# Kernel optimization log

Hardware: AMD Instinct MI355X
Metric: run time of the kernel (lower is better)

The kernel has to match this reference:

```python
import jax, jax.numpy as jnp
import numpy as np

B, H, W, C = 8, 128, 128, 256
IC = C // 8  # im_ch
INF_VAL = 3.4e38  # note: the original ADDS +INF on the H-axis diagonal (as in source)


def setup_inputs() -> dict:
    key = jax.random.key(0)
    ks = jax.random.split(key, 8)
    x = jax.random.normal(ks[0], (B, H, W, C), dtype=jnp.float32)
    s = 1.0 / np.sqrt(C).astype(np.float32)
    Wf = jax.random.normal(ks[1], (C, IC), dtype=jnp.float32) * s
    bf = jnp.zeros((IC,), dtype=jnp.float32)
    Wg = jax.random.normal(ks[2], (C, IC), dtype=jnp.float32) * s
    bg = jnp.zeros((IC,), dtype=jnp.float32)
    Wh = jax.random.normal(ks[3], (C, C), dtype=jnp.float32) * s
    bh = jnp.zeros((C,), dtype=jnp.float32)
    gamma = jnp.float32(0.5)  # source inits to 0.0; use 0.5 so output != x for testing
    return {"x": x, "Wf": Wf, "bf": bf, "Wg": Wg, "bg": bg, "Wh": Wh, "bh": bh, "gamma": gamma}


def reference(x, Wf, bf, Wg, bg, Wh, bh, gamma):
    b, h, w, c = x.shape
    # 1x1 convs == per-pixel GEMMs
    fx = jnp.einsum('bhwc,ck->bhwk', x, Wf) + bf   # [B,H,W,IC]
    gx = jnp.einsum('bhwc,ck->bhwk', x, Wg) + bg   # [B,H,W,IC]
    hx = jnp.einsum('bhwc,cd->bhwd', x, Wh) + bh   # [B,H,W,C]
    # H-axis energy: eh[b,i,w,j] = <fx[b,i,w,:], gx[b,j,w,:]> + INF on i==j diagonal
    eye_bias = (INF_VAL * jnp.eye(h, dtype=x.dtype))[:, None, :]  # [H,1,H] -> broadcast over w
    eh = jnp.einsum('biwk,bjwk->biwj', fx, gx) + eye_bias          # [B,H,W,H]
    # W-axis energy: ew[b,h,i,j] = <fx[b,h,i,:], gx[b,h,j,:]>
    ew = jnp.einsum('bhik,bhjk->bhij', fx, gx)                     # [B,H,W,W]
    # joint softmax over concatenated H+W axis
    att = jax.nn.softmax(jnp.concatenate([eh, ew], axis=-1), axis=-1)  # [B,H,W,H+W]
    att_h, att_w = att[..., :h], att[..., h:]
    # aggregate values along column (H) and row (W)
    out_h = jnp.einsum('biwj,bjwc->biwc', att_h, hx)  # [B,H,W,C]
    out_w = jnp.einsum('bhij,bhjc->bhic', att_w, hx)  # [B,H,W,C]
    return gamma * (out_h + out_w) + x
```

## Files before the change

### kernel.cpp

```cpp
#include <hip/hip_runtime.h>
#include <hip/hip_bf16.h>

typedef __attribute__((ext_vector_type(8))) short bf16x8;
typedef __attribute__((ext_vector_type(4))) float f32x4;

__device__ __forceinline__ unsigned f2bf(float f) {
    union { float f; unsigned u; } v; v.f = f;
    unsigned u = v.u;
    return (u + 0x7FFFu + ((u >> 16) & 1u)) >> 16;
}

__global__ void prep_whT(const float* __restrict__ Wh, ushort* __restrict__ whT) {
    int n = blockIdx.x;
    int k = threadIdx.x;
    whT[n * 256 + k] = (ushort)f2bf(Wh[k * 256 + n]);
}

__global__ __launch_bounds__(256, 4) void ccsa_gemm(
    const float* __restrict__ x, const ushort* __restrict__ whT,
    const float* __restrict__ bh, const float* __restrict__ gamma,
    float* __restrict__ out)
{
    __shared__ char lds[32768];
    const int tid  = threadIdx.x;
    const int lane = tid & 63;
    const int wv   = tid >> 6;
    const int r15  = lane & 15;
    const int g    = lane >> 4;
    const int swz  = (r15 & 7) << 4;

    const long row0 = (long)blockIdx.x * 64;
    const float* xblk = x + row0 * 256;

#pragma unroll
    for (int p = 0; p < 8; ++p) {
        int lin = p * 2048 + tid * 8;
        int r = lin >> 8;
        int c = lin & 255;
        float4 a0 = *(const float4*)(xblk + lin);
        float4 a1 = *(const float4*)(xblk + lin + 4);
        uint4 pk;
        pk.x = f2bf(a0.x) | (f2bf(a0.y) << 16);
        pk.y = f2bf(a0.z) | (f2bf(a0.w) << 16);
        pk.z = f2bf(a1.x) | (f2bf(a1.y) << 16);
        pk.w = f2bf(a1.z) | (f2bf(a1.w) << 16);
        int addr = r * 512 + ((c * 2) ^ ((r & 7) << 4));
        *(uint4*)(lds + addr) = pk;
    }

    const ushort* bp0 = whT + (wv * 64 +  0 + r15) * 256 + g * 8;
    const ushort* bp1 = whT + (wv * 64 + 16 + r15) * 256 + g * 8;
    const ushort* bp2 = whT + (wv * 64 + 32 + r15) * 256 + g * 8;
    const ushort* bp3 = whT + (wv * 64 + 48 + r15) * 256 + g * 8;

    __syncthreads();

    f32x4 acc[4][4] = {};

#pragma unroll
    for (int ksl = 0; ksl < 8; ++ksl) {
        bf16x8 bc[4];
        bc[0] = *(const bf16x8*)(bp0 + ksl * 32);
        bc[1] = *(const bf16x8*)(bp1 + ksl * 32);
        bc[2] = *(const bf16x8*)(bp2 + ksl * 32);
        bc[3] = *(const bf16x8*)(bp3 + ksl * 32);

        const int ko = (ksl * 64 + g * 16) ^ swz;
        bf16x8 af[4];
#pragma unroll
        for (int mi = 0; mi < 4; ++mi)
            af[mi] = *(const bf16x8*)(lds + (mi * 16 + r15) * 512 + ko);

#pragma unroll
        for (int mi = 0; mi < 4; ++mi)
#pragma unroll
            for (int ni = 0; ni < 4; ++ni)
                acc[mi][ni] = __builtin_amdgcn_mfma_f32_16x16x32_bf16(
                    af[mi], bc[ni], acc[mi][ni], 0, 0, 0);
    }

    const float gm = gamma[0];
    float bias[4];
#pragma unroll
    for (int ni = 0; ni < 4; ++ni) bias[ni] = bh[wv * 64 + ni * 16 + r15];

#pragma unroll
    for (int mi = 0; mi < 4; ++mi) {
#pragma unroll
        for (int rr = 0; rr < 4; ++rr) {
            int row = mi * 16 + g * 4 + rr;
#pragma unroll
            for (int ni = 0; ni < 4; ++ni) {
                int col2 = wv * 128 + ni * 32 + r15 * 2;
                int addr = row * 512 + (col2 ^ ((row & 7) << 4));
                ushort xv = *(const ushort*)(lds + addr);
                float xf = __uint_as_float(((unsigned)xv) << 16);
                float val = gm * (acc[mi][ni][rr] + bias[ni]) + xf;
                out[(row0 + row) * 256 + wv * 64 + ni * 16 + r15] = val;
            }
        }
    }
}

extern "C" void kernel_launch(void* const* d_in, const int* in_sizes, int n_in,
                              void* d_out, int out_size, void* d_ws, size_t ws_size,
                              hipStream_t stream) {
    const float* x  = (const float*)d_in[0];
    const float* Wh = (const float*)d_in[5];
    const float* bh = (const float*)d_in[6];
    const float* gm = (const float*)d_in[7];
    float* out = (float*)d_out;
    ushort* whT = (ushort*)d_ws;

    prep_whT<<<256, 256, 0, stream>>>(Wh, whT);
    ccsa_gemm<<<2048, 256, 0, stream>>>(x, whT, bh, gm, out);
}
```

Before: 70.70 us.

## Make GEMM kernel persistent with register prefetch and vectorized nontemporal stores

Converts the per-tile GEMM launch into a persistent grid where each block loops over several 64-row tiles, prefetching the next tile of x into registers while computing the current one. Swaps MFMA operand order so each lane owns four consecutive output columns, enabling float4 nontemporal stores instead of scalar stores. Also flips the weight-transpose prep indexing so global reads coalesce. The prefetch raises register pressure (launch bounds lowered) and the grid may leave some CUs with uneven tile counts.

Measured after the change: 221.9 us. +213.9%, slower.

```diff
diff --git a/kernel.cpp b/kernel.cpp
--- a/kernel.cpp
+++ b/kernel.cpp
@@ -1,22 +1,23 @@
 #include <hip/hip_runtime.h>
-#include <hip/hip_bf16.h>
 
 typedef __attribute__((ext_vector_type(8))) short bf16x8;
 typedef __attribute__((ext_vector_type(4))) float f32x4;
 
 __device__ __forceinline__ unsigned f2bf(float f) {
     union { float f; unsigned u; } v; v.f = f;
-    unsigned u = v.u;
-    return (u + 0x7FFFu + ((u >> 16) & 1u)) >> 16;
+    return (v.u + 0x7FFFu + ((v.u >> 16) & 1u)) >> 16;
 }
 
 __global__ void prep_whT(const float* __restrict__ Wh, ushort* __restrict__ whT) {
-    int n = blockIdx.x;
-    int k = threadIdx.x;
+    int k = blockIdx.x;
+    int n = threadIdx.x;
     whT[n * 256 + k] = (ushort)f2bf(Wh[k * 256 + n]);
 }
 
-__global__ __launch_bounds__(256, 4) void ccsa_gemm(
+#define NTILE 2048
+#define NBLK  683
+
+__global__ __launch_bounds__(256, 3) void ccsa_gemm(
     const float* __restrict__ x, const ushort* __restrict__ whT,
     const float* __restrict__ bh, const float* __restrict__ gamma,
     float* __restrict__ out)
@@ -27,78 +28,105 @@
     const int wv   = tid >> 6;
     const int r15  = lane & 15;
     const int g    = lane >> 4;
-    const int swz  = (r15 & 7) << 4;
 
-    const long row0 = (long)blockIdx.x * 64;
-    const float* xblk = x + row0 * 256;
+    const float gm = gamma[0];
+
+    const ushort* bp[4];
+#pragma unroll
+    for (int ni = 0; ni < 4; ++ni)
+        bp[ni] = whT + (wv * 64 + ni * 16 + r15) * 256 + g * 8;
+
+    float4 bias4[4];
+#pragma unroll
+    for (int ni = 0; ni < 4; ++ni)
+        bias4[ni] = *(const float4*)(bh + wv * 64 + ni * 16 + g * 4);
+
+    float4 ld[16];
+    long t = blockIdx.x;
+
+    {
+        const float* src = x + t * 16384 + tid * 4;
+#pragma unroll
+        for (int i = 0; i < 16; ++i) ld[i] = *(const float4*)(src + i * 1024);
+    }
+#pragma unroll
+    for (int i = 0; i < 16; ++i) {
+        int row = i * 4 + wv;
+        int addr = row * 512 + ((lane * 8) ^ ((row & 7) << 4));
+        uint2 pk;
+        pk.x = f2bf(ld[i].x) | (f2bf(ld[i].y) << 16);
+        pk.y = f2bf(ld[i].z) | (f2bf(ld[i].w) << 16);
+        *(uint2*)(lds + addr) = pk;
+    }
+    __syncthreads();
+
+    while (true) {
+        const long t2 = t + NBLK;
+        const bool pf = (t2 < NTILE);
+
+        f32x4 acc[4][4] = {};
 
 #pragma unroll
-    for (int p = 0; p < 8; ++p) {
-        int lin = p * 2048 + tid * 8;
-        int r = lin >> 8;
-        int c = lin & 255;
-        float4 a0 = *(const float4*)(xblk + lin);
-        float4 a1 = *(const float4*)(xblk + lin + 4);
-        uint4 pk;
-        pk.x = f2bf(a0.x) | (f2bf(a0.y) << 16);
-        pk.y = f2bf(a0.z) | (f2bf(a0.w) << 16);
-        pk.z = f2bf(a1.x) | (f2bf(a1.y) << 16);
-        pk.w = f2bf(a1.z) | (f2bf(a1.w) << 16);
-        int addr = r * 512 + ((c * 2) ^ ((r & 7) << 4));
-        *(uint4*)(lds + addr) = pk;
-    }
-
-    const ushort* bp0 = whT + (wv * 64 +  0 + r15) * 256 + g * 8;
-    const ushort* bp1 = whT + (wv * 64 + 16 + r15) * 256 + g * 8;
-    const ushort* bp2 = whT + (wv * 64 + 32 + r15) * 256 + g * 8;
-    const ushort* bp3 = whT + (wv * 64 + 48 + r15) * 256 + g * 8;
-
-    __syncthreads();
-
-    f32x4 acc[4][4] = {};
-
-#pragma unroll
-    for (int ksl = 0; ksl < 8; ++ksl) {
-        bf16x8 bc[4];
-        bc[0] = *(const bf16x8*)(bp0 + ksl * 32);
-        bc[1] = *(const bf16x8*)(bp1 + ksl * 32);
-        bc[2] = *(const bf16x8*)(bp2 + ksl * 32);
-        bc[3] = *(const bf16x8*)(bp3 + ksl * 32);
-
-        const int ko = (ksl * 64 + g * 16) ^ swz;
-        bf16x8 af[4];
-#pragma unroll
-        for (int mi = 0; mi < 4; ++mi)
-            af[mi] = *(const bf16x8*)(lds + (mi * 16 + r15) * 512 + ko);
-
-#pragma unroll
-        for (int mi = 0; mi < 4; ++mi)
+        for (int ksl = 0; ksl < 8; ++ksl) {
+            bf16x8 bc[4], af[4];
 #pragma unroll
             for (int ni = 0; ni < 4; ++ni)
-                acc[mi][ni] = __builtin_amdgcn_mfma_f32_16x16x32_bf16(
-                    af[mi], bc[ni], acc[mi][ni], 0, 0, 0);
-    }
+                bc[ni] = *(const bf16x8*)(bp[ni] + ksl * 32);
+            const int ko = (ksl * 64 + g * 16) ^ ((r15 & 7) << 4);
+#pragma unroll
+            for (int mi = 0; mi < 4; ++mi)
+                af[mi] = *(const bf16x8*)(lds + (mi * 16 + r15) * 512 + ko);
+#pragma unroll
+            for (int mi = 0; mi < 4; ++mi)
+#pragma unroll
+                for (int ni = 0; ni < 4; ++ni)
+                    acc[mi][ni] = __builtin_amdgcn_mfma_f32_16x16x32_bf16(
+                        bc[ni], af[mi], acc[mi][ni], 0, 0, 0);
+        }
 
-    const float gm = gamma[0];
-    float bias[4];
+        if (pf) {
+            const float* src = x + t2 * 16384 + tid * 4;
 #pragma unroll
-    for (int ni = 0; ni < 4; ++ni) bias[ni] = bh[wv * 64 + ni * 16 + r15];
+            for (int i = 0; i < 16; ++i) ld[i] = *(const float4*)(src + i * 1024);
+        }
 
+        const long row0 = t * 64;
 #pragma unroll
-    for (int mi = 0; mi < 4; ++mi) {
-#pragma unroll
-        for (int rr = 0; rr < 4; ++rr) {
-            int row = mi * 16 + g * 4 + rr;
+        for (int mi = 0; mi < 4; ++mi) {
+            const int row = mi * 16 + r15;
+            const int rb  = row * 512;
+            const int sw  = (row & 7) << 4;
 #pragma unroll
             for (int ni = 0; ni < 4; ++ni) {
-                int col2 = wv * 128 + ni * 32 + r15 * 2;
-                int addr = row * 512 + (col2 ^ ((row & 7) << 4));
-                ushort xv = *(const ushort*)(lds + addr);
-                float xf = __uint_as_float(((unsigned)xv) << 16);
-                float val = gm * (acc[mi][ni][rr] + bias[ni]) + xf;
-                out[(row0 + row) * 256 + wv * 64 + ni * 16 + r15] = val;
+                const int colb = wv * 128 + ni * 32 + g * 8;
+                uint2 rx = *(const uint2*)(lds + rb + (colb ^ sw));
+                float x0 = __uint_as_float(rx.x << 16);
+                float x1 = __uint_as_float(rx.x & 0xFFFF0000u);
+                float x2 = __uint_as_float(rx.y << 16);
+                float x3 = __uint_as_float(rx.y & 0xFFFF0000u);
+                f32x4 o;
+                o[0] = gm * (acc[mi][ni][0] + bias4[ni].x) + x0;
+                o[1] = gm * (acc[mi][ni][1] + bias4[ni].y) + x1;
+                o[2] = gm * (acc[mi][ni][2] + bias4[ni].z) + x2;
+                o[3] = gm * (acc[mi][ni][3] + bias4[ni].w) + x3;
+                f32x4* dst = (f32x4*)(out + (row0 + row) * 256 + wv * 64 + ni * 16 + g * 4);
+                __builtin_nontemporal_store(o, dst);
             }
         }
+
+        __syncthreads();
+        if (!pf) break;
+#pragma unroll
+        for (int i = 0; i < 16; ++i) {
+            int row = i * 4 + wv;
+            int addr = row * 512 + ((lane * 8) ^ ((row & 7) << 4));
+            uint2 pk;
+            pk.x = f2bf(ld[i].x) | (f2bf(ld[i].y) << 16);
+            pk.y = f2bf(ld[i].z) | (f2bf(ld[i].w) << 16);
+            *(uint2*)(lds + addr) = pk;
+        }
+        __syncthreads();
+        t = t2;
     }
 }
 
@@ -113,5 +141,5 @@
     ushort* whT = (ushort*)d_ws;
 
     prep_whT<<<256, 256, 0, stream>>>(Wh, whT);
-    ccsa_gemm<<<2048, 256, 0, stream>>>(x, whT, bh, gm, out);
+    ccsa_gemm<<<NBLK, 256, 0, stream>>>(x, whT, bh, gm, out);
 }
```
